# Performance work log

Hardware: AMD Instinct MI355X
Metric: run time of the kernel (lower is better)

Reference implementation:

```python
import jax, jax.numpy as jnp
import numpy as np


def conv1x1(x, W, b):
    # x: [B,C,H,W], W: [O,C] (1x1 conv kernel squeezed), b: [O]
    return jnp.einsum('bchw,oc->bohw', x, W) + b[None, :, None, None]


def setup_inputs() -> dict:
    key = jax.random.key(0)
    ks = jax.random.split(key, 16)
    B, C, H, W = 4, 2048, 32, 32
    HID = 256  # gate_strength_fc hidden width
    s = 1.0 / np.sqrt(C)
    x = jax.random.normal(ks[0], (B, C, H, W), dtype=jnp.float32)
    mask = jax.random.uniform(ks[1], (B, 1, H, W)) > 0.8
    use_entropy_gate = jax.random.randint(ks[2], (B,), 0, 2).astype(bool)
    return {
        'x': x,
        'Wq': jax.random.normal(ks[3], (C, C)) * s,
        'bq': jnp.zeros((C,), jnp.float32),
        'Wk': jax.random.normal(ks[4], (C, C)) * s,
        'bk': jnp.zeros((C,), jnp.float32),
        'Wv': jax.random.normal(ks[5], (C, C)) * s,
        'bv': jnp.zeros((C,), jnp.float32),
        'Wg': jax.random.normal(ks[6], (C, C)) * s,
        'bg': jnp.zeros((C,), jnp.float32),
        'W1': jax.random.normal(ks[7], (HID, C)) * s,
        'b1': jnp.zeros((HID,), jnp.float32),
        'W2': jax.random.normal(ks[8], (1, HID)) * (1.0 / np.sqrt(HID)),
        'b2': jnp.zeros((1,), jnp.float32),
        'mask': mask,
        'use_entropy_gate': use_entropy_gate,
    }


def reference(x, Wq, bq, Wk, bk, Wv, bv, Wg, bg, W1, b1, W2, b2, mask, use_entropy_gate):
    B, C, H, W = x.shape
    HW = H * W
    masked_x = x * mask.astype(x.dtype)
    # 1x1 conv projections, flattened over spatial dims
    q = conv1x1(masked_x, Wq, bq).reshape(B, C, HW).transpose(0, 2, 1)  # [B,HW,C]
    k = conv1x1(masked_x, Wk, bk).reshape(B, C, HW)                     # [B,C,HW]
    v = conv1x1(x, Wv, bv).reshape(B, C, HW)                            # [B,C,HW]
    # attention[b,n,m] = softmax_m(q[b,n,:] . k[b,:,m])
    attn = jax.nn.softmax(jnp.einsum('bnc,bcm->bnm', q, k), axis=-1)    # [B,HW,HW]
    # out = bmm(value, attention^T): out[b,c,m] = sum_n v[b,c,n] * attn[b,m,n]
    out = jnp.einsum('bcn,bmn->bcm', v, attn).reshape(B, C, H, W)
    # gate strength head: 2048 -> 256 -> 1, then sigmoid
    gate_strength = jax.nn.sigmoid(conv1x1(jax.nn.relu(conv1x1(x, W1, b1)), W2, b2))  # [B,1,H,W]
    gate = jax.nn.sigmoid(conv1x1(x, Wg, bg))                                          # [B,C,H,W]
    gated = out * gate * gate_strength
    # per-sample select: gated attention output where flag set, else passthrough x
    return jnp.where(use_entropy_gate[:, None, None, None], gated, x)
```

## Files before the change

### kernel.cpp

```cpp
#include <hip/hip_runtime.h>
#include <cstddef>
#include <cstdint>


typedef unsigned int u32;
typedef unsigned short u16;
typedef __attribute__((ext_vector_type(8))) short bf16x8;
typedef __attribute__((ext_vector_type(4))) float f32x4;

#define B_   4
#define C_   2048
#define HW_  1024
#define HID_ 256
#define KP   384
#define NQK  384
#define NVGH 704

#define WAITVM(N) asm volatile("s_waitcnt vmcnt(" #N ")" ::: "memory")
__device__ __forceinline__ void barw() {
  asm volatile("" ::: "memory");
  __builtin_amdgcn_s_barrier();
  asm volatile("" ::: "memory");
}

__device__ __forceinline__ float sigmoidf_(float x) {
  return 1.0f / (1.0f + __expf(-x));
}
__device__ __forceinline__ u16 f2bf(float f) {
  u32 u = __float_as_uint(f);
  return (u16)((u + 0x7FFFu + ((u >> 16) & 1u)) >> 16);
}
__device__ __forceinline__ float bf2f(u16 h) {
  return __uint_as_float(((u32)h) << 16);
}
__device__ __forceinline__ void gld16(void* lds, const void* g) {
  __builtin_amdgcn_global_load_lds(
      (const __attribute__((address_space(1))) u32*)g,
      (__attribute__((address_space(3))) u32*)lds, 16, 0, 0);
}

__device__ __forceinline__ void stage128x32s(u16* lds, const u16* g, int ld, int tid) {
#pragma unroll
  for (int t = 0; t < 2; ++t) {
    int s = tid + t * 256;
    int row = s >> 2;
    int oct = ((s & 3) - (row >> 1)) & 3;
    gld16(lds + (size_t)s * 8, g + (size_t)row * ld + oct * 8);
  }
}
template <int NF>
__device__ __forceinline__ void read_frags_s(const u16* lds, int base, int ln, int kq,
                                             bf16x8* f) {
#pragma unroll
  for (int t = 0; t < NF; ++t) {
    int row = base + t * 16 + ln;
    int oct = (kq + (row >> 1)) & 3;
    f[t] = *(const bf16x8*)(lds + (size_t)row * 32 + oct * 8);
  }
}

__device__ __forceinline__ void stage_qk4(u16* L, const u16* Ah, const u16* Al,
                                          const u16* Bh, const u16* Bl, int k0, int tid) {
  stage128x32s(L,         Ah + k0, C_, tid);
  stage128x32s(L + 4096,  Al + k0, C_, tid);
  stage128x32s(L + 8192,  Bh + k0, C_, tid);
  stage128x32s(L + 12288, Bl + k0, C_, tid);
}
__device__ __forceinline__ void stage_ab2(u16* L, const u16* A, const u16* Bp, int k0,
                                          int lda, int ldb, int tid) {
  stage128x32s(L,        A + k0, lda, tid);
  stage128x32s(L + 4096, Bp + k0, ldb, tid);
}
__device__ __forceinline__ void comp_qk(const u16* L, int wm, int wn, int ln, int kq,
                                        f32x4 (&acc)[4][4]) {
  bf16x8 ah[4], al[4], bh[4], bl[4];
  read_frags_s<4>(L, wm, ln, kq, ah);
  read_frags_s<4>(L + 4096, wm, ln, kq, al);
  read_frags_s<4>(L + 8192, wn, ln, kq, bh);
  read_frags_s<4>(L + 12288, wn, ln, kq, bl);
#pragma unroll
  for (int i = 0; i < 4; ++i)
#pragma unroll
    for (int j = 0; j < 4; ++j) {
      acc[i][j] = __builtin_amdgcn_mfma_f32_16x16x32_bf16(ah[i], bh[j], acc[i][j], 0, 0, 0);
      acc[i][j] = __builtin_amdgcn_mfma_f32_16x16x32_bf16(ah[i], bl[j], acc[i][j], 0, 0, 0);
      acc[i][j] = __builtin_amdgcn_mfma_f32_16x16x32_bf16(al[i], bh[j], acc[i][j], 0, 0, 0);
    }
}
__device__ __forceinline__ void comp_ab(const u16* L, int wm, int wn, int ln, int kq,
                                        f32x4 (&acc)[4][4]) {
  bf16x8 af[4], bg_[4];
  read_frags_s<4>(L, wm, ln, kq, af);
  read_frags_s<4>(L + 4096, wn, ln, kq, bg_);
#pragma unroll
  for (int i = 0; i < 4; ++i)
#pragma unroll
    for (int j = 0; j < 4; ++j)
      acc[i][j] = __builtin_amdgcn_mfma_f32_16x16x32_bf16(af[i], bg_[j], acc[i][j], 0, 0, 0);
}

__global__ __launch_bounds__(256)
void scan_mask(const int* __restrict__ mask, int* __restrict__ idx,
               int* __restrict__ rnk, int* __restrict__ cnt)
{
  const int b = blockIdx.x;
  const int t = threadIdx.x;
  __shared__ int base;
  if (t == 0) base = 0;
  __syncthreads();
  int m0 = t * 4;
  int mv[4], local = 0;
#pragma unroll
  for (int i = 0; i < 4; ++i) { mv[i] = mask[b * HW_ + m0 + i] != 0; local += mv[i]; }
  int my = atomicAdd(&base, local);
#pragma unroll
  for (int i = 0; i < 4; ++i) {
    if (mv[i]) {
      int r = my++;
      if (r < KP) { idx[b * KP + r] = m0 + i; rnk[b * HW_ + m0 + i] = r; }
      else rnk[b * HW_ + m0 + i] = -1;
    } else {
      rnk[b * HW_ + m0 + i] = -1;
    }
  }
  __syncthreads();
  if (t == 0) cnt[b] = min(base, KP);
}

__global__ __launch_bounds__(256)
void transpose_fused(const float* __restrict__ x, u16* __restrict__ xhi,
                     u16* __restrict__ xkh, u16* __restrict__ xkl,
                     const int* __restrict__ rnk, const int* __restrict__ useg,
                     float* __restrict__ sx)
{
  const int b = blockIdx.z;
  if (!useg[b]) return;
  __shared__ float t[32][33];
  const int c0 = blockIdx.y * 32, j0 = blockIdx.x * 32;
  const int tid = threadIdx.x;
  const float* xb = x + ((size_t)b * C_ + c0) * (size_t)HW_ + j0;
  {
    int jj = tid & 31, cs = tid >> 5;
#pragma unroll
    for (int t4 = 0; t4 < 4; ++t4) {
      int c = cs * 4 + t4;
      t[c][jj] = xb[(size_t)c * HW_ + jj];
    }
  }
  __syncthreads();
  int j = tid >> 3, c4 = (tid & 7) * 4;
  float v0 = t[c4 + 0][j], v1 = t[c4 + 1][j], v2 = t[c4 + 2][j], v3 = t[c4 + 3][j];
  ushort4 hv;
  hv.x = f2bf(v0); hv.y = f2bf(v1); hv.z = f2bf(v2); hv.w = f2bf(v3);
  *(ushort4*)(xhi + ((size_t)b * HW_ + j0 + j) * (size_t)C_ + c0 + c4) = hv;
  int r = rnk[b * HW_ + j0 + j];
  if (r >= 0) {
    ushort4 lv;
    lv.x = f2bf(v0 - bf2f(hv.x)); lv.y = f2bf(v1 - bf2f(hv.y));
    lv.z = f2bf(v2 - bf2f(hv.z)); lv.w = f2bf(v3 - bf2f(hv.w));
    size_t o = ((size_t)b * KP + r) * (size_t)C_ + c0 + c4;
    *(ushort4*)(xkh + o) = hv;
    *(ushort4*)(xkl + o) = lv;
  }
  if (tid < 32) {
    float s = 0.f;
#pragma unroll
    for (int jj = 0; jj < 32; ++jj) s += t[tid][jj];
    atomicAdd(&sx[b * C_ + c0 + tid], s);
  }
}

__global__ __launch_bounds__(256)
void cast_all(const float* __restrict__ Wq, const float* __restrict__ Wk,
              const float* __restrict__ Wv, const float* __restrict__ Wg,
              const float* __restrict__ W1,
              u16* __restrict__ Wqkh, u16* __restrict__ Wqkl, u16* __restrict__ Wvgh)
{
  const int reg = blockIdx.y;
  int i = (blockIdx.x * 256 + threadIdx.x) * 4;
  const float* src; u16* dh; u16* dl = nullptr; int n = C_ * C_;
  if (reg == 0)      { src = Wq; dh = Wqkh;              dl = Wqkl; }
  else if (reg == 1) { src = Wk; dh = Wqkh + C_ * C_;    dl = Wqkl + C_ * C_; }
  else if (reg == 2) { src = Wv; dh = Wvgh; }
  else if (reg == 3) { src = Wg; dh = Wvgh + C_ * C_; }
  else               { src = W1; dh = Wvgh + 2 * C_ * C_; n = HID_ * C_; }
  if (i >= n) return;
  float4 v = *(const float4*)(src + i);
  ushort4 h;
  h.x = f2bf(v.x); h.y = f2bf(v.y); h.z = f2bf(v.z); h.w = f2bf(v.w);
  *(ushort4*)(dh + i) = h;
  if (dl) {
    ushort4 l;
    l.x = f2bf(v.x - bf2f(h.x)); l.y = f2bf(v.y - bf2f(h.y));
    l.z = f2bf(v.z - bf2f(h.z)); l.w = f2bf(v.w - bf2f(h.w));
    *(ushort4*)(dl + i) = l;
  }
}

__global__ __launch_bounds__(256)
void sv_matvec(const u16* __restrict__ Wvgh, const float* __restrict__ sx,
               const float* __restrict__ bv, float* __restrict__ sv)
{
  __shared__ float sxl[B_ * C_];
  const int tid = threadIdx.x;
  for (int i = tid; i < B_ * C_ / 4; i += 256)
    ((float4*)sxl)[i] = ((const float4*)sx)[i];
  __syncthreads();
  const int c = blockIdx.x * 4 + (tid >> 6);
  const int lane = tid & 63;
  const u16* wrow = Wvgh + (size_t)c * C_;
  float a0 = 0.f, a1 = 0.f, a2 = 0.f, a3 = 0.f;
#pragma unroll
  for (int it = 0; it < C_ / 512; ++it) {
    int k0 = it * 512 + lane * 8;
    bf16x8 wv = *(const bf16x8*)(wrow + k0);
#pragma unroll
    for (int u = 0; u < 8; ++u) {
      float w = bf2f((u16)wv[u]);
      int k = k0 + u;
      a0 = fmaf(w, sxl[k], a0);
      a1 = fmaf(w, sxl[C_ + k], a1);
      a2 = fmaf(w, sxl[2 * C_ + k], a2);
      a3 = fmaf(w, sxl[3 * C_ + k], a3);
    }
  }
#pragma unroll
  for (int off = 32; off > 0; off >>= 1) {
    a0 += __shfl_down(a0, off);
    a1 += __shfl_down(a1, off);
    a2 += __shfl_down(a2, off);
    a3 += __shfl_down(a3, off);
  }
  if (lane == 0) {
    float bb = (float)HW_ * bv[c];
    sv[0 * C_ + c] = a0 + bb;
    sv[1 * C_ + c] = a1 + bb;
    sv[2 * C_ + c] = a2 + bb;
    sv[3 * C_ + c] = a3 + bb;
  }
}

__global__ __launch_bounds__(256, 2)
void mega2_proj(const u16* __restrict__ Wqkh, const u16* __restrict__ Wqkl,
                const u16* __restrict__ xkh, const u16* __restrict__ xkl,
                const u16* __restrict__ Wvgh, const u16* __restrict__ xhi,
                const float* __restrict__ bq, const float* __restrict__ bk,
                const float* __restrict__ bv, const float* __restrict__ bg,
                const float* __restrict__ b1,
                u16* __restrict__ qTh, u16* __restrict__ qTl,
                u16* __restrict__ kTh, u16* __restrict__ kTl,
                u16* __restrict__ vk2, u16* __restrict__ gate, float* __restrict__ h,
                const int* __restrict__ cnt, const int* __restrict__ useg)
{
  __shared__ u16 lds0[4 * 4096];
  __shared__ u16 lds1[4 * 4096];
  const int tid = threadIdx.x;
  const int w = tid >> 6, lane = tid & 63, ln = lane & 15, kq = lane >> 4;
  const int bid = blockIdx.x;

  if (bid < NQK) {
    const int b = bid & 3;
    if (!useg[b]) return;
    const int rest = bid >> 2;
    const int row0 = (rest / 3) * 128;
    const int col0 = (rest % 3) * 128;
    const int RC = (cnt[b] + 127) & ~127;
    if (col0 >= RC) return;
    const int wm = (w >> 1) * 64, wn = (w & 1) * 64;
    f32x4 acc[4][4];
#pragma unroll
    for (int i = 0; i < 4; ++i)
#pragma unroll
      for (int j = 0; j < 4; ++j) acc[i][j] = (f32x4){0.f, 0.f, 0.f, 0.f};

    const u16* Ahb = Wqkh + (size_t)row0 * C_;
    const u16* Alb = Wqkl + (size_t)row0 * C_;
    const u16* Bhb = xkh + ((size_t)b * KP + col0) * (size_t)C_;
    const u16* Blb = xkl + ((size_t)b * KP + col0) * (size_t)C_;

    stage_qk4(lds0, Ahb, Alb, Bhb, Blb, 0, tid);
    stage_qk4(lds1, Ahb, Alb, Bhb, Blb, 32, tid);
    u16 *Lc = lds0, *Ln = lds1;
    for (int t = 0; t + 2 < 64; ++t) {
      WAITVM(8); barw();
      comp_qk(Lc, wm, wn, ln, kq, acc);
      barw();
      stage_qk4(Lc, Ahb, Alb, Bhb, Blb, (t + 2) * 32, tid);
      u16* tp = Lc; Lc = Ln; Ln = tp;
    }
    WAITVM(8); barw();
    comp_qk(Lc, wm, wn, ln, kq, acc);
    barw();
    { u16* tp = Lc; Lc = Ln; Ln = tp; }
    WAITVM(0); barw();
    comp_qk(Lc, wm, wn, ln, kq, acc);

    const int half = row0 >= C_;
    const float* bias = half ? bk : bq;
    u16* Oh = half ? kTh : qTh;
    u16* Ol = half ? kTl : qTl;
    const int mbase = row0 - (half ? C_ : 0);
#pragma unroll
    for (int i = 0; i < 4; ++i) {
      int m = mbase + wm + i * 16 + kq * 4;
      float b4[4];
#pragma unroll
      for (int r = 0; r < 4; ++r) b4[r] = bias[m + r];
#pragma unroll
      for (int j = 0; j < 4; ++j) {
        int n = col0 + wn + j * 16 + ln;
        float v0 = acc[i][j][0] + b4[0];
        float v1 = acc[i][j][1] + b4[1];
        float v2 = acc[i][j][2] + b4[2];
        float v3 = acc[i][j][3] + b4[3];
        ushort4 hv, lv;
        hv.x = f2bf(v0); lv.x = f2bf(v0 - bf2f(hv.x));
        hv.y = f2bf(v1); lv.y = f2bf(v1 - bf2f(hv.y));
        hv.z = f2bf(v2); lv.z = f2bf(v2 - bf2f(hv.z));
        hv.w = f2bf(v3); lv.w = f2bf(v3 - bf2f(hv.w));
        size_t o = ((size_t)b * KP + n) * (size_t)C_ + m;
        *(ushort4*)(Oh + o) = hv;
        *(ushort4*)(Ol + o) = lv;
      }
    }
  } else {
    const int bid2 = bid - NQK;
    const int b = bid2 / 176;
    int rr = bid2 % 176;
    if (!useg[b]) return;
    int sect, row0, pix0;
    if (rr < 32)       { sect = 0; row0 = (rr >> 1) * 128;            pix0 = (rr & 1) * 128; }
    else if (rr < 160) { sect = 1; rr -= 32;  row0 = C_ + (rr >> 3) * 128;     pix0 = (rr & 7) * 128; }
    else               { sect = 2; rr -= 160; row0 = 2 * C_ + (rr >> 3) * 128; pix0 = (rr & 7) * 128; }
    if (sect == 0) {
      const int KC = (cnt[b] + 127) & ~127;
      if (pix0 >= KC) return;
    }
    const int wm = (w >> 1) * 64, wn = (w & 1) * 64;
    f32x4 acc[4][4];
#pragma unroll
    for (int i = 0; i < 4; ++i)
#pragma unroll
      for (int j = 0; j < 4; ++j) acc[i][j] = (f32x4){0.f, 0.f, 0.f, 0.f};

    const u16* Ab = Wvgh + (size_t)row0 * C_;
    const u16* Bb = (sect == 0) ? (xkh + ((size_t)b * KP + pix0) * (size_t)C_)
                                : (xhi + ((size_t)b * HW_ + pix0) * (size_t)C_);

    stage_ab2(lds0, Ab, Bb, 0, C_, C_, tid);
    stage_ab2(lds1, Ab, Bb, 32, C_, C_, tid);
    u16 *Lc = lds0, *Ln = lds1;
    for (int t = 0; t + 2 < 64; ++t) {
      WAITVM(4); barw();
      comp_ab(Lc, wm, wn, ln, kq, acc);
      barw();
      stage_ab2(Lc, Ab, Bb, (t + 2) * 32, C_, C_, tid);
      u16* tp = Lc; Lc = Ln; Ln = tp;
    }
    WAITVM(4); barw();
    comp_ab(Lc, wm, wn, ln, kq, acc);
    barw();
    { u16* tp = Lc; Lc = Ln; Ln = tp; }
    WAITVM(0); barw();
    comp_ab(Lc, wm, wn, ln, kq, acc);

    const float* bias = (sect == 0) ? bv : (sect == 1 ? bg : b1);
    const int sbase = (sect == 0) ? 0 : (sect == 1 ? C_ : 2 * C_);
#pragma unroll
    for (int i = 0; i < 4; ++i) {
      int ml = row0 - sbase + wm + i * 16 + kq * 4;
      float b4[4];
#pragma unroll
      for (int r = 0; r < 4; ++r) b4[r] = bias[ml + r];
#pragma unroll
      for (int j = 0; j < 4; ++j) {
        int pp = pix0 + wn + j * 16 + ln;
#pragma unroll
        for (int r = 0; r < 4; ++r) {
          float val = acc[i][j][r] + b4[r];
          if (sect == 0) {
            vk2[((size_t)b * C_ + ml + r) * (size_t)KP + pp] = f2bf(val);
          } else if (sect == 1) {
            gate[((size_t)b * C_ + ml + r) * (size_t)HW_ + pp] = f2bf(sigmoidf_(val));
          } else {
            h[((size_t)b * HID_ + ml + r) * (size_t)HW_ + pp] = fmaxf(val, 0.f);
          }
        }
      }
    }
  }
}

__global__ __launch_bounds__(256, 2)
void logits_splitk(const u16* __restrict__ qTh, const u16* __restrict__ qTl,
                   const u16* __restrict__ kTh, const u16* __restrict__ kTl,
                   float* __restrict__ lk, const int* __restrict__ cnt,
                   const int* __restrict__ useg)
{
  const int b = blockIdx.z >> 3, ks = blockIdx.z & 7;
  if (!useg[b]) return;
  const int RC = (cnt[b] + 127) & ~127;
  const int row0 = blockIdx.y * 128, col0 = blockIdx.x * 128;
  if (row0 >= RC || col0 >= RC) return;
  __shared__ u16 lds0[4 * 4096];
  __shared__ u16 lds1[4 * 4096];
  const int tid = threadIdx.x;
  const int w = tid >> 6, lane = tid & 63, ln = lane & 15, kq = lane >> 4;
  const int wm = (w >> 1) * 64, wn = (w & 1) * 64;
  f32x4 acc[4][4];
#pragma unroll
  for (int i = 0; i < 4; ++i)
#pragma unroll
    for (int j = 0; j < 4; ++j) acc[i][j] = (f32x4){0.f, 0.f, 0.f, 0.f};

  const size_t bs = (size_t)b * KP * (size_t)C_;
  const u16* Ahb = qTh + bs + (size_t)row0 * C_;
  const u16* Alb = qTl + bs + (size_t)row0 * C_;
  const u16* Bhb = kTh + bs + (size_t)col0 * C_;
  const u16* Blb = kTl + bs + (size_t)col0 * C_;
  const int kbeg = ks * 256;

  stage_qk4(lds0, Ahb, Alb, Bhb, Blb, kbeg, tid);
  stage_qk4(lds1, Ahb, Alb, Bhb, Blb, kbeg + 32, tid);
  u16 *Lc = lds0, *Ln = lds1;
  for (int t = 0; t + 2 < 8; ++t) {
    WAITVM(8); barw();
    comp_qk(Lc, wm, wn, ln, kq, acc);
    barw();
    stage_qk4(Lc, Ahb, Alb, Bhb, Blb, kbeg + (t + 2) * 32, tid);
    u16* tp = Lc; Lc = Ln; Ln = tp;
  }
  WAITVM(8); barw();
  comp_qk(Lc, wm, wn, ln, kq, acc);
  barw();
  { u16* tp = Lc; Lc = Ln; Ln = tp; }
  WAITVM(0); barw();
  comp_qk(Lc, wm, wn, ln, kq, acc);

#pragma unroll
  for (int i = 0; i < 4; ++i) {
    int m = row0 + wm + i * 16 + kq * 4;
#pragma unroll
    for (int j = 0; j < 4; ++j) {
      int n = col0 + wn + j * 16 + ln;
#pragma unroll
      for (int r = 0; r < 4; ++r)
        atomicAdd(&lk[((size_t)b * KP + m + r) * (size_t)KP + n], acc[i][j][r]);
    }
  }
}

__global__ __launch_bounds__(256)
void softmax_ind(const float* __restrict__ lk, const int* __restrict__ rnk,
                 const int* __restrict__ cnt, const int* __restrict__ useg,
                 u16* __restrict__ attn_k, float* __restrict__ cm)
{
  const int b = blockIdx.y;
  if (!useg[b]) return;
  const int mo = blockIdx.x;
  const int t = threadIdx.x;
  const int r = rnk[b * HW_ + mo];
  if (r < 0) {
    if (t == 0) cm[b * HW_ + mo] = 1.0f / HW_;
    return;
  }
  const int n = cnt[b];
  const float* row = lk + ((size_t)b * KP + r) * (size_t)KP;
  float v0 = -1e30f, v1 = -1e30f;
  if (t < n) v0 = row[t];
  if (t + 256 < n) v1 = row[t + 256];

  float mx = fmaxf(fmaxf(v0, v1), 0.0f);
#pragma unroll
  for (int off = 32; off > 0; off >>= 1) mx = fmaxf(mx, __shfl_down(mx, off));
  __shared__ float red[8];
  const int wid = t >> 6;
  if ((t & 63) == 0) red[wid] = mx;
  __syncthreads();
  if (t == 0) red[4] = fmaxf(fmaxf(red[0], red[1]), fmaxf(red[2], red[3]));
  __syncthreads();
  mx = red[4];

  float e0 = (t < n) ? __expf(v0 - mx) : 0.f;
  float e1 = (t + 256 < n) ? __expf(v1 - mx) : 0.f;
  float s = e0 + e1;
#pragma unroll
  for (int off = 32; off > 0; off >>= 1) s += __shfl_down(s, off);
  if ((t & 63) == 0) red[wid] = s;
  __syncthreads();
  if (t == 0) red[5] = red[0] + red[1] + red[2] + red[3] + (HW_ - n) * __expf(-mx);
  __syncthreads();
  float inv = 1.0f / red[5];
  float c = __expf(-mx) * inv;
  if (t == 0) cm[b * HW_ + mo] = c;

  u16* arow = attn_k + ((size_t)b * HW_ + mo) * (size_t)KP;
  if (t < n) arow[t] = f2bf(e0 * inv - c);
  if (t + 256 < n) arow[t + 256] = f2bf(e1 * inv - c);
}

__global__ __launch_bounds__(256)
void gate_strength_k(const float* __restrict__ h, const float* __restrict__ W2,
                     const float* __restrict__ b2, float* __restrict__ gs,
                     const int* __restrict__ useg)
{
  const int b = blockIdx.x >> 4;
  if (!useg[b]) return;
  const int tid = threadIdx.x;
  const int jc = (blockIdx.x & 15) * 64;
  const int j = jc + (tid & 63), is = tid >> 6;
  const float* hb = h + (size_t)b * HID_ * HW_;
  float s = 0.f;
  for (int i = is; i < HID_; i += 4) s = fmaf(W2[i], hb[(size_t)i * HW_ + j], s);
  __shared__ float red[4][64];
  red[is][tid & 63] = s;
  __syncthreads();
  if (is == 0) {
    float tot = red[0][tid] + red[1][tid] + red[2][tid] + red[3][tid];
    gs[(size_t)b * HW_ + j] = sigmoidf_(tot + b2[0]);
  }
}

__global__ __launch_bounds__(256, 2)
void out_compact(const u16* __restrict__ vk2, const u16* __restrict__ attn_k,
                 const float* __restrict__ cm, const float* __restrict__ sv,
                 const u16* __restrict__ gate, const float* __restrict__ gs,
                 const float* __restrict__ x, const int* __restrict__ cnt,
                 const int* __restrict__ useg, float* __restrict__ Out)
{
  const int b = blockIdx.z;
  const int tid = threadIdx.x;
  const int row0 = blockIdx.y * 128, col0 = blockIdx.x * 128;
  if (!useg[b]) {
    const float* xb = x + ((size_t)b * C_ + row0) * (size_t)HW_ + col0;
    float* ob = Out + ((size_t)b * C_ + row0) * (size_t)HW_ + col0;
#pragma unroll
    for (int t = 0; t < 16; ++t) {
      int i2 = tid + t * 256;
      int r = i2 >> 5, c4 = (i2 & 31) * 4;
      *(float4*)(ob + (size_t)r * HW_ + c4) = *(const float4*)(xb + (size_t)r * HW_ + c4);
    }
    return;
  }
  __shared__ u16 lds0[2 * 4096];
  __shared__ u16 lds1[2 * 4096];
  const int w = tid >> 6, lane = tid & 63, ln = lane & 15, kq = lane >> 4;
  const int wm = (w >> 1) * 64, wn = (w & 1) * 64;
  f32x4 acc[4][4];
#pragma unroll
  for (int i = 0; i < 4; ++i)
#pragma unroll
    for (int j = 0; j < 4; ++j) acc[i][j] = (f32x4){0.f, 0.f, 0.f, 0.f};

  const int KR = (cnt[b] + 31) & ~31;
  const int NT = KR / 32;
  const u16* Ab = vk2 + ((size_t)b * C_ + row0) * (size_t)KP;
  const u16* Bb = attn_k + ((size_t)b * HW_ + col0) * (size_t)KP;

  stage_ab2(lds0, Ab, Bb, 0, KP, KP, tid);
  if (NT > 1) stage_ab2(lds1, Ab, Bb, 32, KP, KP, tid);
  u16 *Lc = lds0, *Ln = lds1;
  for (int t = 0; t + 2 < NT; ++t) {
    WAITVM(4); barw();
    comp_ab(Lc, wm, wn, ln, kq, acc);
    barw();
    stage_ab2(Lc, Ab, Bb, (t + 2) * 32, KP, KP, tid);
    u16* tp = Lc; Lc = Ln; Ln = tp;
  }
  if (NT > 1) {
    WAITVM(4); barw();
    comp_ab(Lc, wm, wn, ln, kq, acc);
    barw();
    u16* tp = Lc; Lc = Ln; Ln = tp;
  }
  WAITVM(0); barw();
  comp_ab(Lc, wm, wn, ln, kq, acc);

#pragma unroll
  for (int i = 0; i < 4; ++i) {
    int c = row0 + wm + i * 16 + kq * 4;
    float sv4[4];
#pragma unroll
    for (int r = 0; r < 4; ++r) sv4[r] = sv[(size_t)b * C_ + c + r];
#pragma unroll
    for (int j = 0; j < 4; ++j) {
      int m = col0 + wn + j * 16 + ln;
      float cmv = cm[(size_t)b * HW_ + m];
      float gsv = gs[(size_t)b * HW_ + m];
#pragma unroll
      for (int r = 0; r < 4; ++r) {
        size_t off = ((size_t)b * C_ + c + r) * (size_t)HW_ + m;
        float val = acc[i][j][r] + cmv * sv4[r];
        Out[off] = val * bf2f(gate[off]) * gsv;
      }
    }
  }
}

extern "C" void kernel_launch(void* const* d_in, const int* in_sizes, int n_in,
                              void* d_out, int out_size, void* d_ws, size_t ws_size,
                              hipStream_t stream)
{
  (void)in_sizes; (void)n_in; (void)out_size; (void)ws_size;

  const float* x  = (const float*)d_in[0];
  const float* Wq = (const float*)d_in[1];
  const float* bq = (const float*)d_in[2];
  const float* Wk = (const float*)d_in[3];
  const float* bk = (const float*)d_in[4];
  const float* Wv = (const float*)d_in[5];
  const float* bv = (const float*)d_in[6];
  const float* Wg = (const float*)d_in[7];
  const float* bg = (const float*)d_in[8];
  const float* W1 = (const float*)d_in[9];
  const float* b1 = (const float*)d_in[10];
  const float* W2 = (const float*)d_in[11];
  const float* b2 = (const float*)d_in[12];
  const int* mask = (const int*)d_in[13];
  const int* useg = (const int*)d_in[14];
  float* out = (float*)d_out;

  char* p = (char*)d_ws;
  const size_t SZ_T  = (size_t)B_ * HW_ * C_ * sizeof(u16);
  const size_t SZ_W  = (size_t)2 * C_ * C_ * sizeof(u16);
  const size_t SZ_VG = ((size_t)2 * C_ + HID_) * C_ * sizeof(u16);
  const size_t SZ_XK = (size_t)B_ * KP * C_ * sizeof(u16);

  u16* xhi  = (u16*)p; p += SZ_T;
  u16* Wqkh = (u16*)p; p += SZ_W;
  u16* Wqkl = (u16*)p; p += SZ_W;
  u16* Wvgh = (u16*)p; p += SZ_VG;
  u16* xkh  = (u16*)p; p += SZ_XK;
  u16* xkl  = (u16*)p; p += SZ_XK;
  u16* qTh  = (u16*)p; p += SZ_XK;
  u16* qTl  = (u16*)p; p += SZ_XK;
  u16* kTh  = (u16*)p; p += SZ_XK;
  u16* kTl  = (u16*)p; p += SZ_XK;
  u16* gate = (u16*)p; p += SZ_T;
  u16* vk2  = (u16*)p; p += (size_t)B_ * C_ * KP * sizeof(u16);
  float* h  = (float*)p; p += (size_t)B_ * HID_ * HW_ * sizeof(float);
  float* cm = (float*)p; p += (size_t)B_ * HW_ * sizeof(float);
  float* sv = (float*)p; p += (size_t)B_ * C_ * sizeof(float);
  float* gs = (float*)p; p += (size_t)B_ * HW_ * sizeof(float);
  float* sx = (float*)p; p += (size_t)B_ * C_ * sizeof(float);
  int* idx = (int*)p; p += (size_t)B_ * KP * sizeof(int);
  int* rnk = (int*)p; p += (size_t)B_ * HW_ * sizeof(int);
  int* cnt = (int*)p; p += 64;

  float* lk     = (float*)Wqkh;
  u16*   attn_k = (u16*)((char*)Wqkh + (size_t)B_ * KP * KP * 4);

  dim3 blk(256);

  scan_mask<<<dim3(B_), blk, 0, stream>>>(mask, idx, rnk, cnt);
  hipMemsetAsync(xkh, 0, SZ_XK, stream);
  hipMemsetAsync(xkl, 0, SZ_XK, stream);
  hipMemsetAsync(sx, 0, (size_t)B_ * C_ * sizeof(float), stream);
  transpose_fused<<<dim3(HW_ / 32, C_ / 32, B_), blk, 0, stream>>>(
      x, xhi, xkh, xkl, rnk, useg, sx);
  cast_all<<<dim3(4096, 5), blk, 0, stream>>>(Wq, Wk, Wv, Wg, W1, Wqkh, Wqkl, Wvgh);
  sv_matvec<<<dim3(C_ / 4), blk, 0, stream>>>(Wvgh, sx, bv, sv);

  mega2_proj<<<dim3(NQK + NVGH), blk, 0, stream>>>(
      Wqkh, Wqkl, xkh, xkl, Wvgh, xhi, bq, bk, bv, bg, b1,
      qTh, qTl, kTh, kTl, vk2, gate, h, cnt, useg);

  hipMemsetAsync(lk, 0, (size_t)B_ * KP * KP * sizeof(float), stream);
  hipMemsetAsync(attn_k, 0, (size_t)B_ * HW_ * KP * sizeof(u16), stream);

  logits_splitk<<<dim3(KP / 128, KP / 128, B_ * 8), blk, 0, stream>>>(
      qTh, qTl, kTh, kTl, lk, cnt, useg);

  softmax_ind<<<dim3(HW_, B_), blk, 0, stream>>>(lk, rnk, cnt, useg, attn_k, cm);

  gate_strength_k<<<dim3(B_ * 16), blk, 0, stream>>>(h, W2, b2, gs, useg);

  out_compact<<<dim3(HW_ / 128, C_ / 128, B_), blk, 0, stream>>>(
      vk2, attn_k, cm, sv, gate, gs, x, cnt, useg, out);
}
```

Baseline: 357.0 us.

## Deepen VGH projection pipeline to four LDS stages and interleave block order

Merges the two shared buffers into one 64KB LDS array. The VGH-section GEMM blocks now use a four-stage ring instead of double buffering, keeping three tiles of global loads in flight to hide memory latency. Block indices are also remapped round-robin so that QK and VGH blocks interleave across the grid, which is meant to balance load. The larger shared footprint may limit how many blocks fit on each CU.

```diff
diff --git a/kernel.cpp b/kernel.cpp
--- a/kernel.cpp
+++ b/kernel.cpp
@@ -252,13 +252,14 @@
                 u16* __restrict__ vk2, u16* __restrict__ gate, float* __restrict__ h,
                 const int* __restrict__ cnt, const int* __restrict__ useg)
 {
-  __shared__ u16 lds0[4 * 4096];
-  __shared__ u16 lds1[4 * 4096];
+  __shared__ u16 lds[32768];
   const int tid = threadIdx.x;
   const int w = tid >> 6, lane = tid & 63, ln = lane & 15, kq = lane >> 4;
-  const int bid = blockIdx.x;
+  const int bid = (blockIdx.x & 7) * ((NQK + NVGH) / 8) + (blockIdx.x >> 3);
 
   if (bid < NQK) {
+    u16* L0 = lds;
+    u16* L1 = lds + 16384;
     const int b = bid & 3;
     if (!useg[b]) return;
     const int rest = bid >> 2;
@@ -278,9 +279,9 @@
     const u16* Bhb = xkh + ((size_t)b * KP + col0) * (size_t)C_;
     const u16* Blb = xkl + ((size_t)b * KP + col0) * (size_t)C_;
 
-    stage_qk4(lds0, Ahb, Alb, Bhb, Blb, 0, tid);
-    stage_qk4(lds1, Ahb, Alb, Bhb, Blb, 32, tid);
-    u16 *Lc = lds0, *Ln = lds1;
+    stage_qk4(L0, Ahb, Alb, Bhb, Blb, 0, tid);
+    stage_qk4(L1, Ahb, Alb, Bhb, Blb, 32, tid);
+    u16 *Lc = L0, *Ln = L1;
     for (int t = 0; t + 2 < 64; ++t) {
       WAITVM(8); barw();
       comp_qk(Lc, wm, wn, ln, kq, acc);
@@ -324,6 +325,10 @@
       }
     }
   } else {
+    u16* V0 = lds;
+    u16* V1 = lds + 8192;
+    u16* V2 = lds + 16384;
+    u16* V3 = lds + 24576;
     const int bid2 = bid - NQK;
     const int b = bid2 / 176;
     int rr = bid2 % 176;
@@ -347,22 +352,32 @@
     const u16* Bb = (sect == 0) ? (xkh + ((size_t)b * KP + pix0) * (size_t)C_)
                                 : (xhi + ((size_t)b * HW_ + pix0) * (size_t)C_);
 
-    stage_ab2(lds0, Ab, Bb, 0, C_, C_, tid);
-    stage_ab2(lds1, Ab, Bb, 32, C_, C_, tid);
-    u16 *Lc = lds0, *Ln = lds1;
-    for (int t = 0; t + 2 < 64; ++t) {
-      WAITVM(4); barw();
-      comp_ab(Lc, wm, wn, ln, kq, acc);
+    stage_ab2(V0, Ab, Bb, 0,  C_, C_, tid);
+    stage_ab2(V1, Ab, Bb, 32, C_, C_, tid);
+    stage_ab2(V2, Ab, Bb, 64, C_, C_, tid);
+    stage_ab2(V3, Ab, Bb, 96, C_, C_, tid);
+    for (int t = 0; t < 60; t += 4) {
+      WAITVM(12); barw();
+      comp_ab(V0, wm, wn, ln, kq, acc);
       barw();
-      stage_ab2(Lc, Ab, Bb, (t + 2) * 32, C_, C_, tid);
-      u16* tp = Lc; Lc = Ln; Ln = tp;
-    }
-    WAITVM(4); barw();
-    comp_ab(Lc, wm, wn, ln, kq, acc);
-    barw();
-    { u16* tp = Lc; Lc = Ln; Ln = tp; }
-    WAITVM(0); barw();
-    comp_ab(Lc, wm, wn, ln, kq, acc);
+      stage_ab2(V0, Ab, Bb, (t + 4) * 32, C_, C_, tid);
+      WAITVM(12); barw();
+      comp_ab(V1, wm, wn, ln, kq, acc);
+      barw();
+      stage_ab2(V1, Ab, Bb, (t + 5) * 32, C_, C_, tid);
+      WAITVM(12); barw();
+      comp_ab(V2, wm, wn, ln, kq, acc);
+      barw();
+      stage_ab2(V2, Ab, Bb, (t + 6) * 32, C_, C_, tid);
+      WAITVM(12); barw();
+      comp_ab(V3, wm, wn, ln, kq, acc);
+      barw();
+      stage_ab2(V3, Ab, Bb, (t + 7) * 32, C_, C_, tid);
+    }
+    WAITVM(12); barw(); comp_ab(V0, wm, wn, ln, kq, acc); barw();
+    WAITVM(8);  barw(); comp_ab(V1, wm, wn, ln, kq, acc); barw();
+    WAITVM(4);  barw(); comp_ab(V2, wm, wn, ln, kq, acc); barw();
+    WAITVM(0);  barw(); comp_ab(V3, wm, wn, ln, kq, acc);
 
     const float* bias = (sect == 0) ? bv : (sect == 1 ? bg : b1);
     const int sbase = (sect == 0) ? 0 : (sect == 1 ? C_ : 2 * C_);
```

New measurement: 367.5 us. +2.9%, slower.
